# Kernel optimization log

Hardware: AMD Instinct MI355X
Metric: run time of the kernel (lower is better)

The kernel has to match this reference:

```python
import jax, jax.numpy as jnp
import numpy as np


def setup_inputs() -> dict:
    key = jax.random.key(0)
    ks = jax.random.split(key, 6)
    B, N1, N2 = 4, 16384, 4096
    C1, C2 = 128, 256
    H1, H2 = 256, 128
    Cin = C1 + C2  # 384
    return {
        "xyz1": jax.random.normal(ks[0], (B, N1, 3), dtype=jnp.float32),
        "xyz2": jax.random.normal(ks[1], (B, N2, 3), dtype=jnp.float32),
        "features1": jax.random.normal(ks[2], (B, N1, C1), dtype=jnp.float32),
        "features2": jax.random.normal(ks[3], (B, N2, C2), dtype=jnp.float32),
        "W1": jax.random.normal(ks[4], (Cin, H1), dtype=jnp.float32) * (1.0 / np.sqrt(Cin)),
        "b1": jnp.zeros((H1,), dtype=jnp.float32),
        "W2": jax.random.normal(ks[5], (H1, H2), dtype=jnp.float32) * (1.0 / np.sqrt(H1)),
        "b2": jnp.zeros((H2,), dtype=jnp.float32),
    }


def reference(xyz1, xyz2, features1, features2, W1, b1, W2, b2):
    # Pairwise squared distances: [B, N1, N2]
    diff = xyz1[:, :, None, :] - xyz2[:, None, :, :]
    dist = jnp.sum(diff * diff, axis=-1)
    # 3 smallest distances (tf.argsort ascending, take first 3)
    neg_d3, idx = jax.lax.top_k(-dist, 3)          # idx: [B, N1, 3]
    d3 = jnp.maximum(-neg_d3, 1e-10)
    w = 1.0 / d3
    w = w / jnp.sum(w, axis=-1, keepdims=True)      # [B, N1, 3]
    # Gather features2 at the 3-NN indices per batch: [B, N1, 3, C2]
    gathered = jax.vmap(lambda f, i: f[i])(features2, idx)
    interp = jnp.sum(gathered * w[..., None], axis=2)  # [B, N1, C2]
    new_features = jnp.concatenate([interp, features1], axis=-1)  # [B, N1, C1+C2]
    # Pointwise MLP (Dense + ReLU, no BN)
    h = jax.nn.relu(jnp.einsum("bnc,ch->bnh", new_features, W1) + b1)
    out = jax.nn.relu(jnp.einsum("bnh,ho->bno", h, W2) + b2)
    return out
```

## Files before the change

kernel.cpp:

```cpp
#include <hip/hip_runtime.h>
#include <hip/hip_bf16.h>

typedef __bf16 bf16_t;
typedef __attribute__((ext_vector_type(8))) __bf16 bf16x8;
typedef __attribute__((ext_vector_type(4))) float f32x4;

#define N1 16384
#define N2 4096
#define C1 128
#define C2 256
#define CIN 384
#define HD1 256
#define HD2 128
#define BDIM 4
#define CHUNK 512
#define NCHUNK 8
#define NCAND 24

__global__ void prep_w(const float* __restrict__ W1, const float* __restrict__ W2,
                       const float* __restrict__ f2,
                       bf16_t* __restrict__ W1t, bf16_t* __restrict__ W2t,
                       bf16_t* __restrict__ f2bf) {
  int tid = blockIdx.x * 256 + threadIdx.x;
  if (tid < CIN * HD1) {
    int k = tid / HD1, n = tid % HD1;
    W1t[n * CIN + k] = (bf16_t)W1[tid];
  }
  if (tid < HD1 * HD2) {
    int k = tid / HD2, n = tid % HD2;
    W2t[n * HD1 + k] = (bf16_t)W2[tid];
  }
  const float4* s4 = (const float4*)f2;
  float4 a = s4[2 * (size_t)tid], b = s4[2 * (size_t)tid + 1];
  bf16x8 o;
  o[0] = (bf16_t)a.x; o[1] = (bf16_t)a.y; o[2] = (bf16_t)a.z; o[3] = (bf16_t)a.w;
  o[4] = (bf16_t)b.x; o[5] = (bf16_t)b.y; o[6] = (bf16_t)b.z; o[7] = (bf16_t)b.w;
  *(bf16x8*)(f2bf + (size_t)tid * 8) = o;
}

__global__ __launch_bounds__(256) void knn_chunk(
    const float* __restrict__ xyz1, const float* __restrict__ xyz2,
    float* __restrict__ candd, int* __restrict__ candj) {
  int b  = blockIdx.y;
  int ck = blockIdx.z;
  int i  = blockIdx.x * 256 + threadIdx.x;
  const float* p = xyz1 + ((size_t)b * N1 + i) * 3;
  float px = p[0], py = p[1], pz = p[2];

  const float* x2b = xyz2 + ((size_t)b * N2 + (size_t)ck * CHUNK) * 3;

  float d0 = 3.4e38f, d1 = 3.4e38f, d2 = 3.4e38f;
  int   j0 = 0, j1 = 0, j2 = 0;

  for (int j = 0; j < CHUNK; j += 16) {
    float c[48];
    const float4* q = (const float4*)(x2b + 3 * j);
#pragma unroll
    for (int t = 0; t < 12; ++t) {
      float4 v = q[t];
      c[4 * t + 0] = v.x; c[4 * t + 1] = v.y; c[4 * t + 2] = v.z; c[4 * t + 3] = v.w;
    }
#pragma unroll
    for (int u = 0; u < 16; ++u) {
      float dx = __fsub_rn(c[3 * u + 0], px);
      float dy = __fsub_rn(c[3 * u + 1], py);
      float dz = __fsub_rn(c[3 * u + 2], pz);
      float d = __fadd_rn(__fadd_rn(__fmul_rn(dx, dx), __fmul_rn(dy, dy)),
                          __fmul_rn(dz, dz));
      int jj = j + u;
      if (d < d2) {
        bool lt0 = d < d0, lt1 = d < d1;
        j2 = lt1 ? j1 : jj;
        j1 = lt0 ? j0 : (lt1 ? jj : j1);
        j0 = lt0 ? jj : j0;
        d2 = __builtin_amdgcn_fmed3f(d, d1, d2);
        d1 = __builtin_amdgcn_fmed3f(d, d0, d1);
        d0 = fminf(d, d0);
      }
    }
  }
  size_t qb = ((size_t)b * N1 + i) * NCAND + (size_t)ck * 3;
  int jbase = ck * CHUNK;
  candd[qb + 0] = d0; candd[qb + 1] = d1; candd[qb + 2] = d2;
  candj[qb + 0] = j0 + jbase; candj[qb + 1] = j1 + jbase; candj[qb + 2] = j2 + jbase;
}

__global__ __launch_bounds__(256, 3) void fused_tail(
    const float* __restrict__ f1, const bf16_t* __restrict__ f2b_,
    const float* __restrict__ candd, const int* __restrict__ candj,
    const bf16_t* __restrict__ W1t, const float* __restrict__ b1,
    const bf16_t* __restrict__ W2t, const float* __restrict__ b2,
    float* __restrict__ out) {
  __shared__ __align__(16) char smem[53248];
  bf16_t* As  = (bf16_t*)smem;
  bf16_t* Bs  = (bf16_t*)(smem + 4096);
  bf16_t* Bs2 = (bf16_t*)smem;
  char*   hs  = smem + 20480;
  float*  mw  = (float*)(smem + 20480);
  int*    mj  = (int*)(smem + 20480 + 768);

  int tid = threadIdx.x;
  int wv = tid >> 6, ln = tid & 63, quad = ln >> 4, lm = ln & 15;
  long row0 = (long)blockIdx.x * 64;

  if (tid < 64) {
    size_t q = row0 + tid;
    const float* cd = candd + q * NCAND;
    const int*   cj = candj + q * NCAND;
    float d0 = 3.4e38f, d1 = 3.4e38f, d2 = 3.4e38f;
    int   j0 = 0, j1 = 0, j2 = 0;
#pragma unroll
    for (int c = 0; c < NCAND; ++c) {
      float d = cd[c]; int j = cj[c];
      bool p0 = d < d0, p1 = d < d1, p2 = d < d2;
      j2 = p1 ? j1 : (p2 ? j : j2);
      j1 = p0 ? j0 : (p1 ? j : j1);
      j0 = p0 ? j : j0;
      d2 = __builtin_amdgcn_fmed3f(d, d1, d2);
      d1 = __builtin_amdgcn_fmed3f(d, d0, d1);
      d0 = fminf(d, d0);
    }
    d0 = fmaxf(d0, 1e-10f); d1 = fmaxf(d1, 1e-10f); d2 = fmaxf(d2, 1e-10f);
    float w0 = 1.0f / d0, w1 = 1.0f / d1, w2 = 1.0f / d2;
    float ws = w0 + w1 + w2;
    mw[tid * 3 + 0] = w0 / ws; mw[tid * 3 + 1] = w1 / ws; mw[tid * 3 + 2] = w2 / ws;
    mj[tid * 3 + 0] = j0; mj[tid * 3 + 1] = j1; mj[tid * 3 + 2] = j2;
  }
  __syncthreads();

  int srow = tid >> 2, sh = tid & 3;
  long q = row0 + srow;
  int  b = (int)(q >> 14);
  float u0 = mw[srow * 3 + 0], u1 = mw[srow * 3 + 1], u2 = mw[srow * 3 + 2];
  const bf16_t* f2bb = f2b_ + (size_t)b * N2 * C2;
  const bf16_t* r0p = f2bb + (size_t)mj[srow * 3 + 0] * C2;
  const bf16_t* r1p = f2bb + (size_t)mj[srow * 3 + 1] * C2;
  const bf16_t* r2p = f2bb + (size_t)mj[srow * 3 + 2] * C2;
  const float* f1r = f1 + (size_t)q * C1;
  bf16_t* asd = As + srow * 32 + sh * 8;
  __syncthreads();

  int wn = wv * 64;
  f32x4 acc[4][4] = {};

  bf16x8 g0, g1, g2;
  float4 gfa, gfb;
  {
    int cb = sh * 8;
    g0 = *(const bf16x8*)(r0p + cb);
    g1 = *(const bf16x8*)(r1p + cb);
    g2 = *(const bf16x8*)(r2p + cb);
  }

  for (int ks = 0; ks < 12; ++ks) {
    int kb = ks * 32;
#pragma unroll
    for (int s = 0; s < 4; ++s) {
      __builtin_amdgcn_global_load_lds(
          (const __attribute__((address_space(1))) void*)(
              W1t + (size_t)(wv * 64 + ln) * CIN + kb + s * 8),
          (__attribute__((address_space(3))) void*)(Bs + s * 2048 + wv * 512),
          16, 0, 0);
    }
    bf16x8 o;
    if (ks < 8) {
#pragma unroll
      for (int e = 0; e < 8; ++e)
        o[e] = (bf16_t)(u0 * (float)g0[e] + u1 * (float)g1[e] + u2 * (float)g2[e]);
    } else {
      o[0] = (bf16_t)gfa.x; o[1] = (bf16_t)gfa.y;
      o[2] = (bf16_t)gfa.z; o[3] = (bf16_t)gfa.w;
      o[4] = (bf16_t)gfb.x; o[5] = (bf16_t)gfb.y;
      o[6] = (bf16_t)gfb.z; o[7] = (bf16_t)gfb.w;
    }
    *(bf16x8*)(asd) = o;
    __syncthreads();

    if (ks < 7) {
      int cb = (ks + 1) * 32 + sh * 8;
      g0 = *(const bf16x8*)(r0p + cb);
      g1 = *(const bf16x8*)(r1p + cb);
      g2 = *(const bf16x8*)(r2p + cb);
    } else if (ks < 11) {
      int cf = (ks - 7) * 32 + sh * 8;
      gfa = *(const float4*)(f1r + cf);
      gfb = *(const float4*)(f1r + cf + 4);
    }

    bf16x8 af[4];
#pragma unroll
    for (int mi = 0; mi < 4; ++mi)
      af[mi] = *(const bf16x8*)(As + (mi * 16 + lm) * 32 + quad * 8);
    bf16x8 bfr[4];
#pragma unroll
    for (int ni = 0; ni < 4; ++ni)
      bfr[ni] = *(const bf16x8*)(Bs + quad * 2048 + (wn + ni * 16 + lm) * 8);
#pragma unroll
    for (int mi = 0; mi < 4; ++mi)
#pragma unroll
      for (int ni = 0; ni < 4; ++ni)
        acc[mi][ni] = __builtin_amdgcn_mfma_f32_16x16x32_bf16(af[mi], bfr[ni],
                                                              acc[mi][ni], 0, 0, 0);
    __syncthreads();
  }

#pragma unroll
  for (int mi = 0; mi < 4; ++mi)
#pragma unroll
    for (int ni = 0; ni < 4; ++ni) {
      int col = wn + ni * 16 + lm;
      float bv = b1[col];
#pragma unroll
      for (int r = 0; r < 4; ++r) {
        int row = mi * 16 + quad * 4 + r;
        float v = acc[mi][ni][r] + bv;
        v = fmaxf(v, 0.0f);
        int byte = (row * 512 + col * 2) ^ ((row & 7) << 4);
        *(bf16_t*)(hs + byte) = (bf16_t)v;
      }
    }
  __syncthreads();

  f32x4 acc2[8] = {};
  for (int k0 = 0; k0 < HD1; k0 += 32) {
#pragma unroll
    for (int s = 0; s < 2; ++s) {
      int idx = s * 256 + wv * 64 + ln;
      __builtin_amdgcn_global_load_lds(
          (const __attribute__((address_space(1))) void*)(
              W2t + (size_t)(idx & 127) * HD1 + k0 + (idx >> 7) * 8),
          (__attribute__((address_space(3))) void*)(Bs2 + (s * 256 + wv * 64) * 8),
          16, 0, 0);
    }
    __syncthreads();

    int hrow = wv * 16 + lm;
    bf16x8 af2 = *(const bf16x8*)(
        hs + ((hrow * 512 + (k0 + quad * 8) * 2) ^ ((lm & 7) << 4)));
    bf16x8 bfr2[8];
#pragma unroll
    for (int ni = 0; ni < 8; ++ni)
      bfr2[ni] = *(const bf16x8*)(Bs2 + (quad * 128 + ni * 16 + lm) * 8);
#pragma unroll
    for (int ni = 0; ni < 8; ++ni)
      acc2[ni] = __builtin_amdgcn_mfma_f32_16x16x32_bf16(af2, bfr2[ni],
                                                         acc2[ni], 0, 0, 0);
    __syncthreads();
  }

#pragma unroll
  for (int ni = 0; ni < 8; ++ni) {
    int col = ni * 16 + lm;
    float bv = b2[col];
#pragma unroll
    for (int r = 0; r < 4; ++r) {
      long rowg = row0 + wv * 16 + quad * 4 + r;
      float v = acc2[ni][r] + bv;
      v = fmaxf(v, 0.0f);
      out[rowg * HD2 + col] = v;
    }
  }
}

extern "C" void kernel_launch(void* const* d_in, const int* in_sizes, int n_in,
                              void* d_out, int out_size, void* d_ws, size_t ws_size,
                              hipStream_t stream) {
  const float* xyz1 = (const float*)d_in[0];
  const float* xyz2 = (const float*)d_in[1];
  const float* f1   = (const float*)d_in[2];
  const float* f2   = (const float*)d_in[3];
  const float* W1   = (const float*)d_in[4];
  const float* b1   = (const float*)d_in[5];
  const float* W2   = (const float*)d_in[6];
  const float* b2   = (const float*)d_in[7];
  float* out = (float*)d_out;

  const size_t NQ = (size_t)BDIM * N1;
  char* ws = (char*)d_ws;
  bf16_t* W1t  = (bf16_t*)ws;
  bf16_t* W2t  = (bf16_t*)(ws + (256 << 10));
  bf16_t* f2bf = (bf16_t*)(ws + (512 << 10));
  float*  candd = (float*)(ws + (10 << 20));
  int*    candj = (int*)(ws + (17 << 20));

  prep_w<<<dim3(2048), dim3(256), 0, stream>>>(W1, W2, f2, W1t, W2t, f2bf);
  knn_chunk<<<dim3(N1 / 256, BDIM, NCHUNK), dim3(256), 0, stream>>>(
      xyz1, xyz2, candd, candj);
  fused_tail<<<dim3(NQ / 64), dim3(256), 0, stream>>>(
      f1, f2bf, candd, candj, W1t, b1, W2t, b2, out);
}
```

Before: 263.5 us.

## Split fused tail into 128-row interp+GEMM1 kernel and separate GEMM2

Replaces the single fused interpolation+MLP kernel with two kernels. The first uses 512-thread blocks over 128 rows, doing the 3-NN merge, interpolation and first GEMM, then writes the hidden activations to a global bf16 buffer. The second is a generic 128x128 tiled MFMA GEMM for the second layer. The larger row tile halves how often W1 is re-streamed per block and removes the small serial GEMM2 stage. The cost is an extra round trip of the hidden tensor through global memory and one more launch.

```diff
diff --git a/kernel.cpp b/kernel.cpp
--- a/kernel.cpp
+++ b/kernel.cpp
@@ -85,28 +85,24 @@
   candj[qb + 0] = j0 + jbase; candj[qb + 1] = j1 + jbase; candj[qb + 2] = j2 + jbase;
 }
 
-__global__ __launch_bounds__(256, 3) void fused_tail(
+__global__ __launch_bounds__(512, 4) void interp_gemm1(
     const float* __restrict__ f1, const bf16_t* __restrict__ f2b_,
     const float* __restrict__ candd, const int* __restrict__ candj,
     const bf16_t* __restrict__ W1t, const float* __restrict__ b1,
-    const bf16_t* __restrict__ W2t, const float* __restrict__ b2,
-    float* __restrict__ out) {
-  __shared__ __align__(16) char smem[53248];
-  bf16_t* As  = (bf16_t*)smem;
-  bf16_t* Bs  = (bf16_t*)(smem + 4096);
-  bf16_t* Bs2 = (bf16_t*)smem;
-  char*   hs  = smem + 20480;
-  float*  mw  = (float*)(smem + 20480);
-  int*    mj  = (int*)(smem + 20480 + 768);
-
-  int tid = threadIdx.x;
-  int wv = tid >> 6, ln = tid & 63, quad = ln >> 4, lm = ln & 15;
-  long row0 = (long)blockIdx.x * 64;
-
-  if (tid < 64) {
-    size_t q = row0 + tid;
-    const float* cd = candd + q * NCAND;
-    const int*   cj = candj + q * NCAND;
+    bf16_t* __restrict__ Hbuf) {
+  __shared__ __align__(16) bf16_t As[128 * 32];
+  __shared__ __align__(16) bf16_t Bs[4 * 256 * 8];
+  __shared__ float mw[128 * 3];
+  __shared__ int   mj[128 * 3];
+  int tid  = threadIdx.x;
+  int wv   = tid >> 6, ln = tid & 63;
+  int quad = ln >> 4, lm = ln & 15;
+  long row0 = (long)blockIdx.x * 128;
+
+  if (tid < 128) {
+    size_t qq = row0 + tid;
+    const float* cd = candd + qq * NCAND;
+    const int*   cj = candj + qq * NCAND;
     float d0 = 3.4e38f, d1 = 3.4e38f, d2 = 3.4e38f;
     int   j0 = 0, j1 = 0, j2 = 0;
 #pragma unroll
@@ -138,9 +134,8 @@
   const bf16_t* r2p = f2bb + (size_t)mj[srow * 3 + 2] * C2;
   const float* f1r = f1 + (size_t)q * C1;
   bf16_t* asd = As + srow * 32 + sh * 8;
-  __syncthreads();
-
-  int wn = wv * 64;
+
+  int wm = (wv >> 2) * 64, wn = (wv & 3) * 64;
   f32x4 acc[4][4] = {};
 
   bf16x8 g0, g1, g2;
@@ -155,11 +150,14 @@
   for (int ks = 0; ks < 12; ++ks) {
     int kb = ks * 32;
 #pragma unroll
-    for (int s = 0; s < 4; ++s) {
+    for (int s = 0; s < 2; ++s) {
+      int koct = s * 2 + (wv >> 2);
+      int n    = (wv & 3) * 64 + ln;
       __builtin_amdgcn_global_load_lds(
           (const __attribute__((address_space(1))) void*)(
-              W1t + (size_t)(wv * 64 + ln) * CIN + kb + s * 8),
-          (__attribute__((address_space(3))) void*)(Bs + s * 2048 + wv * 512),
+              W1t + (size_t)n * CIN + kb + koct * 8),
+          (__attribute__((address_space(3))) void*)(
+              Bs + koct * 2048 + (wv & 3) * 512),
           16, 0, 0);
     }
     bf16x8 o;
@@ -190,7 +188,7 @@
     bf16x8 af[4];
 #pragma unroll
     for (int mi = 0; mi < 4; ++mi)
-      af[mi] = *(const bf16x8*)(As + (mi * 16 + lm) * 32 + quad * 8);
+      af[mi] = *(const bf16x8*)(As + (wm + mi * 16 + lm) * 32 + quad * 8);
     bf16x8 bfr[4];
 #pragma unroll
     for (int ni = 0; ni < 4; ++ni)
@@ -212,54 +210,77 @@
       float bv = b1[col];
 #pragma unroll
       for (int r = 0; r < 4; ++r) {
-        int row = mi * 16 + quad * 4 + r;
+        long rowg = row0 + wm + mi * 16 + quad * 4 + r;
         float v = acc[mi][ni][r] + bv;
         v = fmaxf(v, 0.0f);
-        int byte = (row * 512 + col * 2) ^ ((row & 7) << 4);
-        *(bf16_t*)(hs + byte) = (bf16_t)v;
+        Hbuf[rowg * HD1 + col] = (bf16_t)v;
       }
     }
-  __syncthreads();
-
-  f32x4 acc2[8] = {};
-  for (int k0 = 0; k0 < HD1; k0 += 32) {
-#pragma unroll
-    for (int s = 0; s < 2; ++s) {
-      int idx = s * 256 + wv * 64 + ln;
+}
+
+template <bool OUT_BF16>
+__global__ __launch_bounds__(256) void gemm_bt(
+    const bf16_t* __restrict__ A, const bf16_t* __restrict__ Bt,
+    const float* __restrict__ bias, void* __restrict__ Cout,
+    int M, int N, int K) {
+  __shared__ __align__(16) bf16_t As[128 * 32];
+  __shared__ __align__(16) bf16_t Bs[128 * 32];
+  int tid  = threadIdx.x;
+  int wv   = tid >> 6, ln = tid & 63;
+  int quad = ln >> 4, lm = ln & 15;
+  long row0 = (long)blockIdx.x * 128;
+  int  col0 = blockIdx.y * 128;
+  const bf16_t* Ab = A + row0 * K;
+  const bf16_t* Bb = Bt + (long)col0 * K;
+  f32x4 acc[4][4] = {};
+  int wm = (wv >> 1) * 64, wn = (wv & 1) * 64;
+
+  for (int k0 = 0; k0 < K; k0 += 32) {
+#pragma unroll
+    for (int t = 0; t < 2; ++t) {
+      int c = t * 256 + tid;
+      int r = c >> 2, kc = (c & 3) << 3;
       __builtin_amdgcn_global_load_lds(
-          (const __attribute__((address_space(1))) void*)(
-              W2t + (size_t)(idx & 127) * HD1 + k0 + (idx >> 7) * 8),
-          (__attribute__((address_space(3))) void*)(Bs2 + (s * 256 + wv * 64) * 8),
+          (const __attribute__((address_space(1))) void*)(Ab + (long)r * K + k0 + kc),
+          (__attribute__((address_space(3))) void*)(As + (t * 256 + wv * 64) * 8),
           16, 0, 0);
+      __builtin_amdgcn_global_load_lds(
+          (const __attribute__((address_space(1))) void*)(Bb + (long)r * K + k0 + kc),
+          (__attribute__((address_space(3))) void*)(Bs + (t * 256 + wv * 64) * 8),
+          16, 0, 0);
     }
     __syncthreads();
-
-    int hrow = wv * 16 + lm;
-    bf16x8 af2 = *(const bf16x8*)(
-        hs + ((hrow * 512 + (k0 + quad * 8) * 2) ^ ((lm & 7) << 4)));
-    bf16x8 bfr2[8];
-#pragma unroll
-    for (int ni = 0; ni < 8; ++ni)
-      bfr2[ni] = *(const bf16x8*)(Bs2 + (quad * 128 + ni * 16 + lm) * 8);
-#pragma unroll
-    for (int ni = 0; ni < 8; ++ni)
-      acc2[ni] = __builtin_amdgcn_mfma_f32_16x16x32_bf16(af2, bfr2[ni],
-                                                         acc2[ni], 0, 0, 0);
+    bf16x8 af[4], bfr[4];
+#pragma unroll
+    for (int mi = 0; mi < 4; ++mi)
+      af[mi] = *(const bf16x8*)(As + (wm + mi * 16 + lm) * 32 + quad * 8);
+#pragma unroll
+    for (int ni = 0; ni < 4; ++ni)
+      bfr[ni] = *(const bf16x8*)(Bs + (wn + ni * 16 + lm) * 32 + quad * 8);
+#pragma unroll
+    for (int mi = 0; mi < 4; ++mi)
+#pragma unroll
+      for (int ni = 0; ni < 4; ++ni)
+        acc[mi][ni] = __builtin_amdgcn_mfma_f32_16x16x32_bf16(af[mi], bfr[ni],
+                                                              acc[mi][ni], 0, 0, 0);
     __syncthreads();
   }
 
 #pragma unroll
-  for (int ni = 0; ni < 8; ++ni) {
-    int col = ni * 16 + lm;
-    float bv = b2[col];
-#pragma unroll
-    for (int r = 0; r < 4; ++r) {
-      long rowg = row0 + wv * 16 + quad * 4 + r;
-      float v = acc2[ni][r] + bv;
-      v = fmaxf(v, 0.0f);
-      out[rowg * HD2 + col] = v;
-    }
-  }
+  for (int mi = 0; mi < 4; ++mi)
+#pragma unroll
+    for (int ni = 0; ni < 4; ++ni) {
+      int col = col0 + wn + ni * 16 + lm;
+      float bv = bias[col];
+#pragma unroll
+      for (int r = 0; r < 4; ++r) {
+        long rowg = row0 + wm + mi * 16 + quad * 4 + r;
+        float v = acc[mi][ni][r] + bv;
+        v = fmaxf(v, 0.0f);
+        if (OUT_BF16) ((bf16_t*)Cout)[rowg * N + col] = (bf16_t)v;
+        else          ((float*)Cout)[rowg * N + col]  = v;
+      }
+    }
 }
 
 extern "C" void kernel_launch(void* const* d_in, const int* in_sizes, int n_in,
@@ -281,11 +302,14 @@
   bf16_t* W2t  = (bf16_t*)(ws + (256 << 10));
   bf16_t* f2bf = (bf16_t*)(ws + (512 << 10));
   float*  candd = (float*)(ws + (10 << 20));
-  int*    candj = (int*)(ws + (17 << 20));
+  int*    candj = (int*)(ws + (23 << 20));
+  bf16_t* Hbuf  = (bf16_t*)(ws + (36 << 20));
 
   prep_w<<<dim3(2048), dim3(256), 0, stream>>>(W1, W2, f2, W1t, W2t, f2bf);
   knn_chunk<<<dim3(N1 / 256, BDIM, NCHUNK), dim3(256), 0, stream>>>(
       xyz1, xyz2, candd, candj);
-  fused_tail<<<dim3(NQ / 64), dim3(256), 0, stream>>>(
-      f1, f2bf, candd, candj, W1t, b1, W2t, b2, out);
-}
+  interp_gemm1<<<dim3(NQ / 128), dim3(512), 0, stream>>>(
+      f1, f2bf, candd, candj, W1t, b1, Hbuf);
+  gemm_bt<false><<<dim3(NQ / 128, HD2 / 128), dim3(256), 0, stream>>>(
+      Hbuf, W2t, b2, (void*)out, NQ, HD2, HD1);
+}
```

Result: no change. 268.1 us (+1.8%).
